# Kernel tuning notes

Measured on AMD Instinct MI355X. Metric: run time of the kernel, lower is better.

Reference implementation:

```python
import jax, jax.numpy as jnp
import numpy as np

D_MODEL = 1024
D_HEAD = 64
N_HEADS = D_MODEL // D_HEAD
MAX_SEQ = 2048
BATCH = 2
SEQ = 2048


def setup_inputs() -> dict:
    key = jax.random.key(0)
    ks = jax.random.split(key, 10)
    s = 1.0 / np.sqrt(D_MODEL)
    return {
        "x": jax.random.normal(ks[0], (BATCH, SEQ, D_MODEL), dtype=jnp.float32),
        "Wq": jax.random.normal(ks[1], (D_MODEL, D_MODEL), dtype=jnp.float32) * s,
        "bq": jax.random.normal(ks[2], (D_MODEL,), dtype=jnp.float32) * 0.01,
        "Wk": jax.random.normal(ks[3], (D_MODEL, D_MODEL), dtype=jnp.float32) * s,
        "bk": jax.random.normal(ks[4], (D_MODEL,), dtype=jnp.float32) * 0.01,
        "Wv": jax.random.normal(ks[5], (D_MODEL, D_MODEL), dtype=jnp.float32) * s,
        "bv": jax.random.normal(ks[6], (D_MODEL,), dtype=jnp.float32) * 0.01,
        "Er": jax.random.normal(ks[7], (MAX_SEQ, D_HEAD), dtype=jnp.float32),
        "Wo": jax.random.normal(ks[8], (D_MODEL, D_MODEL), dtype=jnp.float32) * s,
        "bo": jax.random.normal(ks[9], (D_MODEL,), dtype=jnp.float32) * 0.01,
    }


def _s_rel(q, Er):
    # q: [B,H,S,Dh]; use last S rows of Er (start = max_seq - seq)
    S = q.shape[2]
    Er_slice = Er[Er.shape[0] - S:, :]                  # [S, Dh]
    qE = jnp.einsum("bhsd,ld->bhsl", q, Er_slice)       # [B,H,S,S]
    padded = jnp.pad(qE, ((0, 0), (0, 0), (0, 0), (1, 0)))  # [B,H,S,S+1]
    B, H, S1, S2 = padded.shape
    padded = padded.reshape(B, H, S2, S1)               # skew trick
    return padded[:, :, 1:, :]                          # [B,H,S,S]


def reference(x, Wq, bq, Wk, bk, Wv, bv, Er, Wo, bo):
    B, S, _ = x.shape
    scale = 1.0 / np.sqrt(D_HEAD)
    # projections (torch Linear: x @ W.T + b)
    def proj(W, b):
        return (x @ W.T + b).reshape(B, S, N_HEADS, D_HEAD).transpose(0, 2, 1, 3)
    q = proj(Wq, bq)   # [B,H,S,Dh]
    k = proj(Wk, bk)
    v = proj(Wv, bv)
    qk = jnp.einsum("bhsd,bhtd->bhst", q, k)            # [B,H,S,S]
    logits = (qk + _s_rel(q, Er)) * scale
    causal = jnp.tril(jnp.ones((S, S), dtype=bool))
    masked = jnp.where(causal[None, None], logits, -1e9)
    attn = jax.nn.softmax(masked, axis=-1)
    out = jnp.einsum("bhst,bhtd->bhsd", attn, v)        # [B,H,S,Dh]
    out = out.transpose(0, 2, 1, 3).reshape(B, S, D_MODEL)
    return out @ Wo.T + bo
```

## Files before the change

### kernel.cpp

```cpp
#include <hip/hip_runtime.h>
#include <hip/hip_bf16.h>

typedef short v8s __attribute__((ext_vector_type(8)));
typedef float v4f __attribute__((ext_vector_type(4)));
typedef __hip_bfloat16 bf16;

#define MFMA(a, b, c) __builtin_amdgcn_mfma_f32_16x16x32_bf16(a, b, c, 0, 0, 0)

__global__ __launch_bounds__(256) void cast_all(
    const float* __restrict__ x,  const float* __restrict__ wq,
    const float* __restrict__ wk, const float* __restrict__ wv,
    const float* __restrict__ wo, const float* __restrict__ er,
    bf16* __restrict__ xb,  bf16* __restrict__ wqb, bf16* __restrict__ wkb,
    bf16* __restrict__ wvb, bf16* __restrict__ wob, bf16* __restrict__ erb)
{
    const int r = blockIdx.y;
    const float* s; bf16* d; int n4;
    if      (r == 0) { s = x;  d = xb;  n4 = 1048576; }
    else if (r == 1) { s = wq; d = wqb; n4 = 262144;  }
    else if (r == 2) { s = wk; d = wkb; n4 = 262144;  }
    else if (r == 3) { s = wv; d = wvb; n4 = 262144;  }
    else if (r == 4) { s = wo; d = wob; n4 = 262144;  }
    else             { s = er; d = erb; n4 = 32768;   }
    const int i = blockIdx.x * 256 + threadIdx.x;
    if (i < n4) {
        const float4 v = ((const float4*)s)[i];
        bf16 t[4];
        t[0] = __float2bfloat16(v.x);
        t[1] = __float2bfloat16(v.y);
        t[2] = __float2bfloat16(v.z);
        t[3] = __float2bfloat16(v.w);
        ((uint2*)d)[i] = *(const uint2*)t;
    }
}

__global__ __launch_bounds__(256) void gemm_nt(
    const bf16* __restrict__ A,
    const bf16* __restrict__ W0, const bf16* __restrict__ W1, const bf16* __restrict__ W2,
    const float* __restrict__ b0, const float* __restrict__ b1, const float* __restrict__ b2,
    bf16* __restrict__ o0, bf16* __restrict__ o1, bf16* __restrict__ o2,
    float* __restrict__ outf, int headmajor)
{
    const int z = blockIdx.z;
    const bf16* W     = (z == 0) ? W0 : (z == 1) ? W1 : W2;
    const float* bias = (z == 0) ? b0 : (z == 1) ? b1 : b2;
    bf16* out         = (z == 0) ? o0 : (z == 1) ? o1 : o2;

    __shared__ bf16 As[128 * 40];
    __shared__ bf16 Bs[128 * 40];

    const int tid = threadIdx.x;
    const int w  = tid >> 6, l = tid & 63;
    const int lm = l & 15,  lq = l >> 4;
    const int wm = (w >> 1) * 64, wn = (w & 1) * 64;
    const int m0 = blockIdx.y * 128, n0 = blockIdx.x * 128;

    v4f acc[4][4];
#pragma unroll
    for (int i = 0; i < 4; ++i)
#pragma unroll
        for (int j = 0; j < 4; ++j) acc[i][j] = (v4f){0.f, 0.f, 0.f, 0.f};

    const int r0 = tid >> 2;
    const int c8 = (tid & 3) * 8;

    for (int k0 = 0; k0 < 1024; k0 += 32) {
        __syncthreads();
#pragma unroll
        for (int rep = 0; rep < 2; ++rep) {
            const int row = r0 + rep * 64;
            *(uint4*)&As[row * 40 + c8] = *(const uint4*)&A[(size_t)(m0 + row) * 1024 + k0 + c8];
            *(uint4*)&Bs[row * 40 + c8] = *(const uint4*)&W[(size_t)(n0 + row) * 1024 + k0 + c8];
        }
        __syncthreads();
        v8s a[4], b[4];
#pragma unroll
        for (int i = 0; i < 4; ++i) a[i] = *(const v8s*)&As[(wm + i * 16 + lm) * 40 + lq * 8];
#pragma unroll
        for (int j = 0; j < 4; ++j) b[j] = *(const v8s*)&Bs[(wn + j * 16 + lm) * 40 + lq * 8];
#pragma unroll
        for (int i = 0; i < 4; ++i)
#pragma unroll
            for (int j = 0; j < 4; ++j)
                acc[i][j] = MFMA(a[i], b[j], acc[i][j]);
    }

    float bv[4];
#pragma unroll
    for (int j = 0; j < 4; ++j) bv[j] = bias[n0 + wn + j * 16 + lm];

#pragma unroll
    for (int i = 0; i < 4; ++i) {
#pragma unroll
        for (int j = 0; j < 4; ++j) {
            const int col = n0 + wn + j * 16 + lm;
#pragma unroll
            for (int r = 0; r < 4; ++r) {
                const int row = m0 + wm + i * 16 + lq * 4 + r;
                const float v = acc[i][j][r] + bv[j];
                if (headmajor) {
                    const int bb = row >> 11, ss = row & 2047;
                    const int hh = col >> 6,  dd = col & 63;
                    out[((size_t)(bb * 16 + hh) * 2048 + ss) * 64 + dd] = __float2bfloat16(v);
                } else {
                    outf[(size_t)row * 1024 + col] = v;
                }
            }
        }
    }
}

__global__ __launch_bounds__(256) void vtrans(const bf16* __restrict__ V, bf16* __restrict__ Vt)
{
    __shared__ bf16 T[64 * 72];
    const int s0  = blockIdx.x * 64;
    const int bh  = blockIdx.y;
    const int tid = threadIdx.x;
#pragma unroll
    for (int rep = 0; rep < 2; ++rep) {
        const int unit = tid + rep * 256;
        const int sl = unit >> 3, d8 = (unit & 7) * 8;
        *(uint4*)&T[sl * 72 + d8] = *(const uint4*)&V[((size_t)bh * 2048 + s0 + sl) * 64 + d8];
    }
    __syncthreads();
#pragma unroll
    for (int rep = 0; rep < 2; ++rep) {
        const int unit = tid + rep * 256;
        const int d = unit >> 3, t8 = (unit & 7) * 8;
        unsigned short tmp[8];
#pragma unroll
        for (int j = 0; j < 8; ++j) tmp[j] = *(const unsigned short*)&T[(t8 + j) * 72 + d];
        *(uint4*)&Vt[((size_t)bh * 64 + d) * 2048 + s0 + t8] = *(const uint4*)tmp;
    }
}

__global__ __launch_bounds__(256, 4) void attn(
    const bf16* __restrict__ Q, const bf16* __restrict__ K,
    const bf16* __restrict__ Vt, const bf16* __restrict__ Er,
    bf16* __restrict__ AO)
{
    __shared__ bf16 Ks[64 * 72];
    __shared__ bf16 Vs[64 * 72];
    __shared__ bf16 Ps[64 * 72];
    __shared__ bf16 Gs[64 * 84];

    const int ord = blockIdx.x;
    const int u = ord & 255, j = ord >> 8;
    const int a = u & 31, yh = u >> 5;
    const int q1 = (j & 2) ? (a ^ 16) : a;
    const int qb = (j & 1) ? (31 - q1) : q1;
    const int bh = 8 * j + yh;

    const int i0 = qb * 64;
    const int b  = bh >> 4, h = bh & 15;
    const int tid = threadIdx.x;
    const int w  = tid >> 6, l = tid & 63;
    const int lm = l & 15,  lq = l >> 4;

    const bf16* qp = Q + ((size_t)bh * 2048 + i0 + w * 16 + lm) * 64 + lq * 8;
    const v8s q0 = *(const v8s*)qp;
    const v8s q1f = *(const v8s*)(qp + 32);

    v4f accO[4];
#pragma unroll
    for (int dt = 0; dt < 4; ++dt) accO[dt] = (v4f){0.f, 0.f, 0.f, 0.f};
    float rs[4];
#pragma unroll
    for (int r = 0; r < 4; ++r) rs[r] = 0.f;

    const int sr0 = tid >> 3;
    const int sc8 = (tid & 7) * 8;
    const size_t kbase = (size_t)bh * 2048 * 64;
    const size_t vbase = (size_t)bh * 64 * 2048;

    const int nk = qb + 1;

    uint4 kp0 = *(const uint4*)&K[kbase + (size_t)sr0 * 64 + sc8];
    uint4 kp1 = *(const uint4*)&K[kbase + (size_t)(sr0 + 32) * 64 + sc8];
    uint4 vp0 = *(const uint4*)&Vt[vbase + (size_t)sr0 * 2048 + sc8];
    uint4 vp1 = *(const uint4*)&Vt[vbase + (size_t)(sr0 + 32) * 2048 + sc8];

    for (int it = 0; it < nk; ++it) {
        const int j0 = it * 64;
        __syncthreads();
        *(uint4*)&Ks[sr0 * 72 + sc8]        = kp0;
        *(uint4*)&Ks[(sr0 + 32) * 72 + sc8] = kp1;
        *(uint4*)&Vs[sr0 * 72 + sc8]        = vp0;
        *(uint4*)&Vs[(sr0 + 32) * 72 + sc8] = vp1;
        if (it + 1 < nk) {
            const int jn = j0 + 64;
            kp0 = *(const uint4*)&K[kbase + (size_t)(jn + sr0) * 64 + sc8];
            kp1 = *(const uint4*)&K[kbase + (size_t)(jn + sr0 + 32) * 64 + sc8];
            vp0 = *(const uint4*)&Vt[vbase + (size_t)sr0 * 2048 + jn + sc8];
            vp1 = *(const uint4*)&Vt[vbase + (size_t)(sr0 + 32) * 2048 + jn + sc8];
        }
        const int basew = 2048 - 16 - i0 + j0 - 16 * w;
#pragma unroll
        for (int ct2 = 0; ct2 < 5; ++ct2) {
            int mr = basew + ct2 * 16 + lm;
            mr = (mr > 2047) ? 2047 : mr;
            const bf16* ep = Er + (size_t)mr * 64 + lq * 8;
            const v8s e0 = *(const v8s*)ep;
            const v8s e1 = *(const v8s*)(ep + 32);
            v4f g = (v4f){0.f, 0.f, 0.f, 0.f};
            g = MFMA(q0, e0, g);
            g = MFMA(q1f, e1, g);
#pragma unroll
            for (int r = 0; r < 4; ++r)
                Gs[(w * 16 + lq * 4 + r) * 84 + ct2 * 16 + lm] =
                    __float2bfloat16(g[r] * 0.125f);
        }
        __syncthreads();
        v4f sv[4];
#pragma unroll
        for (int ct = 0; ct < 4; ++ct) {
            const v8s k0f = *(const v8s*)&Ks[(ct * 16 + lm) * 72 + lq * 8];
            const v8s k1f = *(const v8s*)&Ks[(ct * 16 + lm) * 72 + 32 + lq * 8];
            v4f s = (v4f){0.f, 0.f, 0.f, 0.f};
            s = MFMA(q0, k0f, s);
            s = MFMA(q1f, k1f, s);
            sv[ct] = s;
        }
#pragma unroll
        for (int r = 0; r < 4; ++r) {
            const int rl = lq * 4 + r;
            const int ig = i0 + w * 16 + rl;
#pragma unroll
            for (int ct = 0; ct < 4; ++ct) {
                const int jj = ct * 16 + lm;
                const float gb = (float)Gs[(w * 16 + rl) * 84 + jj + 15 - rl];
                float s = fmaf(sv[ct][r], 0.125f, gb);
                if (j0 + jj > ig) s = -1e9f;
                const float pe = __expf(s - 4.0f);
                rs[r] += pe;
                Ps[(w * 16 + rl) * 72 + jj] = __float2bfloat16(pe);
            }
        }
        const v8s pa0 = *(const v8s*)&Ps[(w * 16 + lm) * 72 + lq * 8];
        const v8s pa1 = *(const v8s*)&Ps[(w * 16 + lm) * 72 + 32 + lq * 8];
#pragma unroll
        for (int dt = 0; dt < 4; ++dt) {
            const v8s vb0 = *(const v8s*)&Vs[(dt * 16 + lm) * 72 + lq * 8];
            const v8s vb1 = *(const v8s*)&Vs[(dt * 16 + lm) * 72 + 32 + lq * 8];
            accO[dt] = MFMA(pa0, vb0, accO[dt]);
            accO[dt] = MFMA(pa1, vb1, accO[dt]);
        }
    }
#pragma unroll
    for (int r = 0; r < 4; ++r) {
#pragma unroll
        for (int msk = 8; msk >= 1; msk >>= 1)
            rs[r] += __shfl_xor(rs[r], msk, 64);
    }
#pragma unroll
    for (int dt = 0; dt < 4; ++dt) {
#pragma unroll
        for (int r = 0; r < 4; ++r) {
            const int row = i0 + w * 16 + lq * 4 + r;
            const int d   = dt * 16 + lm;
            const float v = accO[dt][r] / rs[r];
            AO[((size_t)b * 2048 + row) * 1024 + h * 64 + d] = __float2bfloat16(v);
        }
    }
}

extern "C" void kernel_launch(void* const* d_in, const int* in_sizes, int n_in,
                              void* d_out, int out_size, void* d_ws, size_t ws_size,
                              hipStream_t stream)
{
    const float* x  = (const float*)d_in[0];
    const float* Wq = (const float*)d_in[1];
    const float* bq = (const float*)d_in[2];
    const float* Wk = (const float*)d_in[3];
    const float* bk = (const float*)d_in[4];
    const float* Wv = (const float*)d_in[5];
    const float* bv = (const float*)d_in[6];
    const float* Er = (const float*)d_in[7];
    const float* Wo = (const float*)d_in[8];
    const float* bo = (const float*)d_in[9];
    float* out = (float*)d_out;

    bf16* ws = (bf16*)d_ws;
    const size_t NEl = (size_t)4096 * 1024;
    bf16* Qw  = ws;
    bf16* Kw  = ws + NEl;
    bf16* Vw  = ws + 2 * NEl;
    bf16* Vtw = ws + 3 * NEl;
    bf16* xb  = ws + 4 * NEl;
    bf16* AOw = xb;
    bf16* Wqb = ws + 5 * NEl;
    bf16* Wkb = Wqb + 1024 * 1024;
    bf16* Wvb = Wkb + 1024 * 1024;
    bf16* Wob = Wvb + 1024 * 1024;
    bf16* Erb = Wob + 1024 * 1024;

    cast_all<<<dim3(4096, 6), 256, 0, stream>>>(x, Wq, Wk, Wv, Wo, Er,
                                                xb, Wqb, Wkb, Wvb, Wob, Erb);
    gemm_nt<<<dim3(8, 32, 3), 256, 0, stream>>>(xb, Wqb, Wkb, Wvb, bq, bk, bv,
                                                Qw, Kw, Vw, nullptr, 1);
    vtrans<<<dim3(32, 32), 256, 0, stream>>>(Vw, Vtw);
    attn<<<dim3(1024), 256, 0, stream>>>(Qw, Kw, Vtw, Erb, AOw);
    gemm_nt<<<dim3(8, 32, 1), 256, 0, stream>>>(AOw, Wob, Wob, Wob, bo, bo, bo,
                                                AOw, AOw, AOw, out, 0);
}
```

Before: 280.7 us.

## Split causal attention KV tiles evenly across blocks with atomic partial accumulation

Replaces the one-query-block-per-workgroup causal schedule with a flattened list of (bh, query block, key tile) work items, split into near-equal chunks of 16–17 tiles per workgroup. Partial unnormalized outputs and row sums go to an fp32 buffer (the output tensor, memset to zero) via atomicAdd when a query block is split, and a new normalize kernel divides and casts to bf16. This targets load imbalance from the triangular causal workload. In exchange it adds memsets, fp32 atomics, an extra kernel and an extra pass over the output. It relies on the fixed softmax shift of 4 rather than a running max, so the partial sums add up correctly.

```diff
diff --git a/kernel.cpp b/kernel.cpp
--- a/kernel.cpp
+++ b/kernel.cpp
@@ -137,131 +137,167 @@
 __global__ __launch_bounds__(256, 4) void attn(
     const bf16* __restrict__ Q, const bf16* __restrict__ K,
     const bf16* __restrict__ Vt, const bf16* __restrict__ Er,
-    bf16* __restrict__ AO)
+    float* __restrict__ Of, float* __restrict__ dsum)
 {
     __shared__ bf16 Ks[64 * 72];
     __shared__ bf16 Vs[64 * 72];
     __shared__ bf16 Ps[64 * 72];
     __shared__ bf16 Gs[64 * 84];
 
-    const int ord = blockIdx.x;
-    const int u = ord & 255, j = ord >> 8;
-    const int a = u & 31, yh = u >> 5;
-    const int q1 = (j & 2) ? (a ^ 16) : a;
-    const int qb = (j & 1) ? (31 - q1) : q1;
-    const int bh = 8 * j + yh;
-
-    const int i0 = qb * 64;
-    const int b  = bh >> 4, h = bh & 15;
     const int tid = threadIdx.x;
     const int w  = tid >> 6, l = tid & 63;
     const int lm = l & 15,  lq = l >> 4;
-
-    const bf16* qp = Q + ((size_t)bh * 2048 + i0 + w * 16 + lm) * 64 + lq * 8;
-    const v8s q0 = *(const v8s*)qp;
-    const v8s q1f = *(const v8s*)(qp + 32);
-
-    v4f accO[4];
-#pragma unroll
-    for (int dt = 0; dt < 4; ++dt) accO[dt] = (v4f){0.f, 0.f, 0.f, 0.f};
-    float rs[4];
-#pragma unroll
-    for (int r = 0; r < 4; ++r) rs[r] = 0.f;
-
     const int sr0 = tid >> 3;
     const int sc8 = (tid & 7) * 8;
-    const size_t kbase = (size_t)bh * 2048 * 64;
-    const size_t vbase = (size_t)bh * 64 * 2048;
-
-    const int nk = qb + 1;
-
-    uint4 kp0 = *(const uint4*)&K[kbase + (size_t)sr0 * 64 + sc8];
-    uint4 kp1 = *(const uint4*)&K[kbase + (size_t)(sr0 + 32) * 64 + sc8];
-    uint4 vp0 = *(const uint4*)&Vt[vbase + (size_t)sr0 * 2048 + sc8];
-    uint4 vp1 = *(const uint4*)&Vt[vbase + (size_t)(sr0 + 32) * 2048 + sc8];
-
-    for (int it = 0; it < nk; ++it) {
-        const int j0 = it * 64;
-        __syncthreads();
-        *(uint4*)&Ks[sr0 * 72 + sc8]        = kp0;
-        *(uint4*)&Ks[(sr0 + 32) * 72 + sc8] = kp1;
-        *(uint4*)&Vs[sr0 * 72 + sc8]        = vp0;
-        *(uint4*)&Vs[(sr0 + 32) * 72 + sc8] = vp1;
-        if (it + 1 < nk) {
-            const int jn = j0 + 64;
-            kp0 = *(const uint4*)&K[kbase + (size_t)(jn + sr0) * 64 + sc8];
-            kp1 = *(const uint4*)&K[kbase + (size_t)(jn + sr0 + 32) * 64 + sc8];
-            vp0 = *(const uint4*)&Vt[vbase + (size_t)sr0 * 2048 + jn + sc8];
-            vp1 = *(const uint4*)&Vt[vbase + (size_t)(sr0 + 32) * 2048 + jn + sc8];
-        }
-        const int basew = 2048 - 16 - i0 + j0 - 16 * w;
-#pragma unroll
-        for (int ct2 = 0; ct2 < 5; ++ct2) {
-            int mr = basew + ct2 * 16 + lm;
-            mr = (mr > 2047) ? 2047 : mr;
-            const bf16* ep = Er + (size_t)mr * 64 + lq * 8;
-            const v8s e0 = *(const v8s*)ep;
-            const v8s e1 = *(const v8s*)(ep + 32);
-            v4f g = (v4f){0.f, 0.f, 0.f, 0.f};
-            g = MFMA(q0, e0, g);
-            g = MFMA(q1f, e1, g);
-#pragma unroll
-            for (int r = 0; r < 4; ++r)
-                Gs[(w * 16 + lq * 4 + r) * 84 + ct2 * 16 + lm] =
-                    __float2bfloat16(g[r] * 0.125f);
-        }
-        __syncthreads();
-        v4f sv[4];
-#pragma unroll
-        for (int ct = 0; ct < 4; ++ct) {
-            const v8s k0f = *(const v8s*)&Ks[(ct * 16 + lm) * 72 + lq * 8];
-            const v8s k1f = *(const v8s*)&Ks[(ct * 16 + lm) * 72 + 32 + lq * 8];
-            v4f s = (v4f){0.f, 0.f, 0.f, 0.f};
-            s = MFMA(q0, k0f, s);
-            s = MFMA(q1f, k1f, s);
-            sv[ct] = s;
+
+    const int ord = blockIdx.x;
+    int g = ord * 16 + ((ord + 1) >> 1);
+    const int gend = g + ((ord & 1) ? 16 : 17);
+
+    while (g < gend) {
+        const int bh  = g / 528;
+        const int rem = g - bh * 528;
+        int qb = (int)((sqrtf(8.f * (float)rem + 1.f) - 1.f) * 0.5f);
+        while ((qb + 1) * (qb + 2) / 2 <= rem) ++qb;
+        while (qb * (qb + 1) / 2 > rem) --qb;
+        const int t0 = rem - (qb * (qb + 1)) / 2;
+        int nt = qb + 1 - t0;
+        if (nt > gend - g) nt = gend - g;
+
+        const int i0 = qb * 64;
+        const int b  = bh >> 4, h = bh & 15;
+
+        const bf16* qp = Q + ((size_t)bh * 2048 + i0 + w * 16 + lm) * 64 + lq * 8;
+        const v8s q0  = *(const v8s*)qp;
+        const v8s q1f = *(const v8s*)(qp + 32);
+
+        v4f accO[4];
+#pragma unroll
+        for (int dt = 0; dt < 4; ++dt) accO[dt] = (v4f){0.f, 0.f, 0.f, 0.f};
+        float rs[4] = {0.f, 0.f, 0.f, 0.f};
+
+        const size_t kbase = (size_t)bh * 2048 * 64;
+        const size_t vbase = (size_t)bh * 64 * 2048;
+        const int jt0 = t0 * 64;
+
+        uint4 kp0 = *(const uint4*)&K[kbase + (size_t)(jt0 + sr0) * 64 + sc8];
+        uint4 kp1 = *(const uint4*)&K[kbase + (size_t)(jt0 + sr0 + 32) * 64 + sc8];
+        uint4 vp0 = *(const uint4*)&Vt[vbase + (size_t)sr0 * 2048 + jt0 + sc8];
+        uint4 vp1 = *(const uint4*)&Vt[vbase + (size_t)(sr0 + 32) * 2048 + jt0 + sc8];
+
+        for (int tt = 0; tt < nt; ++tt) {
+            const int jt = jt0 + tt * 64;
+            __syncthreads();
+            *(uint4*)&Ks[sr0 * 72 + sc8]        = kp0;
+            *(uint4*)&Ks[(sr0 + 32) * 72 + sc8] = kp1;
+            *(uint4*)&Vs[sr0 * 72 + sc8]        = vp0;
+            *(uint4*)&Vs[(sr0 + 32) * 72 + sc8] = vp1;
+            if (tt + 1 < nt) {
+                const int jn = jt + 64;
+                kp0 = *(const uint4*)&K[kbase + (size_t)(jn + sr0) * 64 + sc8];
+                kp1 = *(const uint4*)&K[kbase + (size_t)(jn + sr0 + 32) * 64 + sc8];
+                vp0 = *(const uint4*)&Vt[vbase + (size_t)sr0 * 2048 + jn + sc8];
+                vp1 = *(const uint4*)&Vt[vbase + (size_t)(sr0 + 32) * 2048 + jn + sc8];
+            }
+            const int basew = 2048 - 16 - i0 + jt - 16 * w;
+#pragma unroll
+            for (int ct2 = 0; ct2 < 5; ++ct2) {
+                int mr = basew + ct2 * 16 + lm;
+                mr = (mr > 2047) ? 2047 : mr;
+                const bf16* ep = Er + (size_t)mr * 64 + lq * 8;
+                const v8s e0 = *(const v8s*)ep;
+                const v8s e1 = *(const v8s*)(ep + 32);
+                v4f gg = (v4f){0.f, 0.f, 0.f, 0.f};
+                gg = MFMA(q0, e0, gg);
+                gg = MFMA(q1f, e1, gg);
+#pragma unroll
+                for (int r = 0; r < 4; ++r)
+                    Gs[(w * 16 + lq * 4 + r) * 84 + ct2 * 16 + lm] =
+                        __float2bfloat16(gg[r] * 0.125f);
+            }
+            __syncthreads();
+            v4f sv[4];
+#pragma unroll
+            for (int ct = 0; ct < 4; ++ct) {
+                const v8s k0f = *(const v8s*)&Ks[(ct * 16 + lm) * 72 + lq * 8];
+                const v8s k1f = *(const v8s*)&Ks[(ct * 16 + lm) * 72 + 32 + lq * 8];
+                v4f s = (v4f){0.f, 0.f, 0.f, 0.f};
+                s = MFMA(q0, k0f, s);
+                s = MFMA(q1f, k1f, s);
+                sv[ct] = s;
+            }
+#pragma unroll
+            for (int r = 0; r < 4; ++r) {
+                const int rl = lq * 4 + r;
+                const int ig = i0 + w * 16 + rl;
+#pragma unroll
+                for (int ct = 0; ct < 4; ++ct) {
+                    const int jj = ct * 16 + lm;
+                    const float gb = (float)Gs[(w * 16 + rl) * 84 + jj + 15 - rl];
+                    float s = fmaf(sv[ct][r], 0.125f, gb);
+                    if (jt + jj > ig) s = -1e9f;
+                    const float pe = __expf(s - 4.0f);
+                    rs[r] += pe;
+                    Ps[(w * 16 + rl) * 72 + jj] = __float2bfloat16(pe);
+                }
+            }
+            const v8s pa0 = *(const v8s*)&Ps[(w * 16 + lm) * 72 + lq * 8];
+            const v8s pa1 = *(const v8s*)&Ps[(w * 16 + lm) * 72 + 32 + lq * 8];
+#pragma unroll
+            for (int dt = 0; dt < 4; ++dt) {
+                const v8s vb0 = *(const v8s*)&Vs[(dt * 16 + lm) * 72 + lq * 8];
+                const v8s vb1 = *(const v8s*)&Vs[(dt * 16 + lm) * 72 + 32 + lq * 8];
+                accO[dt] = MFMA(pa0, vb0, accO[dt]);
+                accO[dt] = MFMA(pa1, vb1, accO[dt]);
+            }
         }
 #pragma unroll
         for (int r = 0; r < 4; ++r) {
-            const int rl = lq * 4 + r;
-            const int ig = i0 + w * 16 + rl;
-#pragma unroll
-            for (int ct = 0; ct < 4; ++ct) {
-                const int jj = ct * 16 + lm;
-                const float gb = (float)Gs[(w * 16 + rl) * 84 + jj + 15 - rl];
-                float s = fmaf(sv[ct][r], 0.125f, gb);
-                if (j0 + jj > ig) s = -1e9f;
-                const float pe = __expf(s - 4.0f);
-                rs[r] += pe;
-                Ps[(w * 16 + rl) * 72 + jj] = __float2bfloat16(pe);
-            }
-        }
-        const v8s pa0 = *(const v8s*)&Ps[(w * 16 + lm) * 72 + lq * 8];
-        const v8s pa1 = *(const v8s*)&Ps[(w * 16 + lm) * 72 + 32 + lq * 8];
+#pragma unroll
+            for (int msk = 8; msk >= 1; msk >>= 1)
+                rs[r] += __shfl_xor(rs[r], msk, 64);
+        }
+        const bool full = (t0 == 0) && (nt == qb + 1);
 #pragma unroll
         for (int dt = 0; dt < 4; ++dt) {
-            const v8s vb0 = *(const v8s*)&Vs[(dt * 16 + lm) * 72 + lq * 8];
-            const v8s vb1 = *(const v8s*)&Vs[(dt * 16 + lm) * 72 + 32 + lq * 8];
-            accO[dt] = MFMA(pa0, vb0, accO[dt]);
-            accO[dt] = MFMA(pa1, vb1, accO[dt]);
-        }
-    }
-#pragma unroll
-    for (int r = 0; r < 4; ++r) {
-#pragma unroll
-        for (int msk = 8; msk >= 1; msk >>= 1)
-            rs[r] += __shfl_xor(rs[r], msk, 64);
-    }
-#pragma unroll
-    for (int dt = 0; dt < 4; ++dt) {
-#pragma unroll
-        for (int r = 0; r < 4; ++r) {
-            const int row = i0 + w * 16 + lq * 4 + r;
-            const int d   = dt * 16 + lm;
-            const float v = accO[dt][r] / rs[r];
-            AO[((size_t)b * 2048 + row) * 1024 + h * 64 + d] = __float2bfloat16(v);
-        }
-    }
+#pragma unroll
+            for (int r = 0; r < 4; ++r) {
+                const int row = i0 + w * 16 + lq * 4 + r;
+                const int d   = dt * 16 + lm;
+                const size_t idx = ((size_t)b * 2048 + row) * 1024 + h * 64 + d;
+                if (full) Of[idx] = accO[dt][r];
+                else      atomicAdd(&Of[idx], accO[dt][r]);
+            }
+        }
+        if (lm == 0) {
+#pragma unroll
+            for (int r = 0; r < 4; ++r) {
+                const int row = i0 + w * 16 + lq * 4 + r;
+                if (full) dsum[bh * 2048 + row] = rs[r];
+                else      atomicAdd(&dsum[bh * 2048 + row], rs[r]);
+            }
+        }
+        g += nt;
+    }
+}
+
+__global__ __launch_bounds__(256) void normalize(
+    const float* __restrict__ Of, const float* __restrict__ dsum,
+    bf16* __restrict__ AO)
+{
+    const int i = blockIdx.x * 256 + threadIdx.x;
+    const float4 v = ((const float4*)Of)[i];
+    const int e   = i * 4;
+    const int row = e >> 10;
+    const int hh  = (e >> 6) & 15;
+    const int bb  = row >> 11, ss = row & 2047;
+    const float inv = 1.0f / dsum[(size_t)(bb * 16 + hh) * 2048 + ss];
+    bf16 t[4];
+    t[0] = __float2bfloat16(v.x * inv);
+    t[1] = __float2bfloat16(v.y * inv);
+    t[2] = __float2bfloat16(v.z * inv);
+    t[3] = __float2bfloat16(v.w * inv);
+    ((uint2*)AO)[i] = *(const uint2*)t;
 }
 
 extern "C" void kernel_launch(void* const* d_in, const int* in_sizes, int n_in,
@@ -293,13 +329,18 @@
     bf16* Wvb = Wkb + 1024 * 1024;
     bf16* Wob = Wvb + 1024 * 1024;
     bf16* Erb = Wob + 1024 * 1024;
+    float* dsumf = (float*)(Erb + (size_t)2048 * 64);
+
+    hipMemsetAsync(out,   0, NEl * sizeof(float), stream);
+    hipMemsetAsync(dsumf, 0, (size_t)32 * 2048 * sizeof(float), stream);
 
     cast_all<<<dim3(4096, 6), 256, 0, stream>>>(x, Wq, Wk, Wv, Wo, Er,
                                                 xb, Wqb, Wkb, Wvb, Wob, Erb);
     gemm_nt<<<dim3(8, 32, 3), 256, 0, stream>>>(xb, Wqb, Wkb, Wvb, bq, bk, bv,
                                                 Qw, Kw, Vw, nullptr, 1);
     vtrans<<<dim3(32, 32), 256, 0, stream>>>(Vw, Vtw);
-    attn<<<dim3(1024), 256, 0, stream>>>(Qw, Kw, Vtw, Erb, AOw);
+    attn<<<dim3(1024), 256, 0, stream>>>(Qw, Kw, Vtw, Erb, out, dsumf);
+    normalize<<<dim3(4096), 256, 0, stream>>>(out, dsumf, AOw);
     gemm_nt<<<dim3(8, 32, 1), 256, 0, stream>>>(AOw, Wob, Wob, Wob, bo, bo, bo,
                                                 AOw, AOw, AOw, out, 0);
 }
```

New measurement: 302.8 us. +7.9%, slower.

## Use direct global-to-LDS loads with XOR swizzle and BK=64 in projection GEMM

Applied to the files above, without the earlier changes.

The GEMM now stages tiles with global_load_lds 16-byte direct copies into an XOR-swizzled 128-byte-row LDS layout, which skips the register round trip and avoids bank conflicts. The K step doubles to 64, halving the number of barriers per tile. The three QKV projections are treated as one contiguous N=3072 weight matrix, relying on Wq/Wk/Wv and Q/K/V being adjacent in the workspace. Staging is still single-buffered, so load latency is not overlapped with compute.

```diff
diff --git a/kernel.cpp b/kernel.cpp
--- a/kernel.cpp
+++ b/kernel.cpp
@@ -4,8 +4,15 @@
 typedef short v8s __attribute__((ext_vector_type(8)));
 typedef float v4f __attribute__((ext_vector_type(4)));
 typedef __hip_bfloat16 bf16;
+typedef unsigned int u32;
 
 #define MFMA(a, b, c) __builtin_amdgcn_mfma_f32_16x16x32_bf16(a, b, c, 0, 0, 0)
+
+__device__ __forceinline__ void gload16(const bf16* g, bf16* l) {
+    __builtin_amdgcn_global_load_lds(
+        (const __attribute__((address_space(1))) u32*)(g),
+        (__attribute__((address_space(3))) u32*)(l), 16, 0, 0);
+}
 
 __global__ __launch_bounds__(256) void cast_all(
     const float* __restrict__ x,  const float* __restrict__ wq,
@@ -35,19 +42,13 @@
 }
 
 __global__ __launch_bounds__(256) void gemm_nt(
-    const bf16* __restrict__ A,
-    const bf16* __restrict__ W0, const bf16* __restrict__ W1, const bf16* __restrict__ W2,
-    const float* __restrict__ b0, const float* __restrict__ b1, const float* __restrict__ b2,
-    bf16* __restrict__ o0, bf16* __restrict__ o1, bf16* __restrict__ o2,
-    float* __restrict__ outf, int headmajor)
-{
-    const int z = blockIdx.z;
-    const bf16* W     = (z == 0) ? W0 : (z == 1) ? W1 : W2;
-    const float* bias = (z == 0) ? b0 : (z == 1) ? b1 : b2;
-    bf16* out         = (z == 0) ? o0 : (z == 1) ? o1 : o2;
-
-    __shared__ bf16 As[128 * 40];
-    __shared__ bf16 Bs[128 * 40];
+    const bf16* __restrict__ A, const bf16* __restrict__ W,
+    const float* __restrict__ b0, const float* __restrict__ b1,
+    const float* __restrict__ b2,
+    bf16* __restrict__ oHM, float* __restrict__ outf)
+{
+    __shared__ bf16 As[128 * 64];
+    __shared__ bf16 Bs[128 * 64];
 
     const int tid = threadIdx.x;
     const int w  = tid >> 6, l = tid & 63;
@@ -55,55 +56,72 @@
     const int wm = (w >> 1) * 64, wn = (w & 1) * 64;
     const int m0 = blockIdx.y * 128, n0 = blockIdx.x * 128;
 
+    const int grow = l >> 3;
+    const int gcol = ((l & 7) ^ grow) * 8;
+
     v4f acc[4][4];
 #pragma unroll
     for (int i = 0; i < 4; ++i)
 #pragma unroll
         for (int j = 0; j < 4; ++j) acc[i][j] = (v4f){0.f, 0.f, 0.f, 0.f};
 
-    const int r0 = tid >> 2;
-    const int c8 = (tid & 3) * 8;
-
-    for (int k0 = 0; k0 < 1024; k0 += 32) {
+    const int sw = (lm & 7) << 4;
+
+    for (int k0 = 0; k0 < 1024; k0 += 64) {
         __syncthreads();
 #pragma unroll
-        for (int rep = 0; rep < 2; ++rep) {
-            const int row = r0 + rep * 64;
-            *(uint4*)&As[row * 40 + c8] = *(const uint4*)&A[(size_t)(m0 + row) * 1024 + k0 + c8];
-            *(uint4*)&Bs[row * 40 + c8] = *(const uint4*)&W[(size_t)(n0 + row) * 1024 + k0 + c8];
+        for (int q = 0; q < 4; ++q) {
+            const int rr = w * 32 + q * 8;
+            gload16(&A[(size_t)(m0 + rr + grow) * 1024 + k0 + gcol], &As[rr * 64]);
+            gload16(&W[(size_t)(n0 + rr + grow) * 1024 + k0 + gcol], &Bs[rr * 64]);
         }
         __syncthreads();
-        v8s a[4], b[4];
-#pragma unroll
-        for (int i = 0; i < 4; ++i) a[i] = *(const v8s*)&As[(wm + i * 16 + lm) * 40 + lq * 8];
-#pragma unroll
-        for (int j = 0; j < 4; ++j) b[j] = *(const v8s*)&Bs[(wn + j * 16 + lm) * 40 + lq * 8];
-#pragma unroll
-        for (int i = 0; i < 4; ++i)
-#pragma unroll
-            for (int j = 0; j < 4; ++j)
-                acc[i][j] = MFMA(a[i], b[j], acc[i][j]);
-    }
+#pragma unroll
+        for (int kk = 0; kk < 2; ++kk) {
+            v8s a[4], b[4];
+            const int cb = (lq * 16 + kk * 64);
+#pragma unroll
+            for (int i = 0; i < 4; ++i) {
+                const int row = wm + i * 16 + lm;
+                a[i] = *(const v8s*)((const char*)As + row * 128 + (cb ^ sw));
+            }
+#pragma unroll
+            for (int j = 0; j < 4; ++j) {
+                const int row = wn + j * 16 + lm;
+                b[j] = *(const v8s*)((const char*)Bs + row * 128 + (cb ^ sw));
+            }
+#pragma unroll
+            for (int i = 0; i < 4; ++i)
+#pragma unroll
+                for (int j = 0; j < 4; ++j)
+                    acc[i][j] = MFMA(a[i], b[j], acc[i][j]);
+        }
+    }
+
+    const int z = blockIdx.x >> 3;
+    const float* bias = (z == 0) ? b0 : (z == 1) ? b1 : b2;
 
     float bv[4];
 #pragma unroll
-    for (int j = 0; j < 4; ++j) bv[j] = bias[n0 + wn + j * 16 + lm];
+    for (int j = 0; j < 4; ++j) bv[j] = bias[(n0 & 1023) + wn + j * 16 + lm];
 
 #pragma unroll
     for (int i = 0; i < 4; ++i) {
 #pragma unroll
         for (int j = 0; j < 4; ++j) {
             const int col = n0 + wn + j * 16 + lm;
+            const int cc  = col & 1023;
 #pragma unroll
             for (int r = 0; r < 4; ++r) {
                 const int row = m0 + wm + i * 16 + lq * 4 + r;
                 const float v = acc[i][j][r] + bv[j];
-                if (headmajor) {
+                if (outf) {
+                    outf[(size_t)row * 1024 + cc] = v;
+                } else {
                     const int bb = row >> 11, ss = row & 2047;
-                    const int hh = col >> 6,  dd = col & 63;
-                    out[((size_t)(bb * 16 + hh) * 2048 + ss) * 64 + dd] = __float2bfloat16(v);
-                } else {
-                    outf[(size_t)row * 1024 + col] = v;
+                    const int hh = cc >> 6,  dd = cc & 63;
+                    oHM[(size_t)z * 4194304 +
+                        ((size_t)(bb * 16 + hh) * 2048 + ss) * 64 + dd] = __float2bfloat16(v);
                 }
             }
         }
@@ -293,13 +311,12 @@
     bf16* Wvb = Wkb + 1024 * 1024;
     bf16* Wob = Wvb + 1024 * 1024;
     bf16* Erb = Wob + 1024 * 1024;
+    (void)Kw; (void)Vw; (void)Wkb; (void)Wvb;
 
     cast_all<<<dim3(4096, 6), 256, 0, stream>>>(x, Wq, Wk, Wv, Wo, Er,
                                                 xb, Wqb, Wkb, Wvb, Wob, Erb);
-    gemm_nt<<<dim3(8, 32, 3), 256, 0, stream>>>(xb, Wqb, Wkb, Wvb, bq, bk, bv,
-                                                Qw, Kw, Vw, nullptr, 1);
+    gemm_nt<<<dim3(24, 32), 256, 0, stream>>>(xb, Wqb, bq, bk, bv, Qw, nullptr);
     vtrans<<<dim3(32, 32), 256, 0, stream>>>(Vw, Vtw);
     attn<<<dim3(1024), 256, 0, stream>>>(Qw, Kw, Vtw, Erb, AOw);
-    gemm_nt<<<dim3(8, 32, 1), 256, 0, stream>>>(AOw, Wob, Wob, Wob, bo, bo, bo,
-                                                AOw, AOw, AOw, out, 0);
-}
+    gemm_nt<<<dim3(8, 32), 256, 0, stream>>>(AOw, Wob, bo, bo, bo, nullptr, out);
+}
```

Measured after the change: 278.3 us. About the same (-0.9%).
